# Performance work log

Measured on AMD Instinct MI355X. Metric: run time of the kernel, lower is better.

## Reference

```python
import jax, jax.numpy as jnp
import numpy as np

IMG, P, INC = 384, 2, 3
C = 2 * IMG            # embed_dim = 768
NP_ = IMG // P         # 192 patches
N = NP_ + 1            # 193 tokens with cls
L, H, E, K, B = 6, 12, 8, 2, 32
HD = C // H
EPS = 1e-5


def layer_norm(x, w, b):
    m = jnp.mean(x, -1, keepdims=True)
    v = jnp.mean((x - m) ** 2, -1, keepdims=True)
    return (x - m) * jax.lax.rsqrt(v + EPS) * w + b


def setup_inputs() -> dict:
    key = jax.random.key(0)
    ks = iter(jax.random.split(key, 32))
    nrm = lambda sh, s=0.02: jax.random.normal(next(ks), sh, jnp.float32) * s
    inp = {
        'x1': nrm((B, INC, IMG, IMG), 1.0),
        'x2': nrm((B, INC, IMG, IMG), 1.0),
        'patch_w': nrm((C, INC, IMG, P)),
        'patch_b': jnp.zeros((C,)),
        'cls_token': nrm((1, 1, C), 1e-6),
        'ln1_w': jnp.ones((L, C)), 'ln1_b': jnp.zeros((L, C)),
        'qkv_w': nrm((L, 3 * C, C)), 'qkv_b': jnp.zeros((L, 3 * C)),
        'proj_w': nrm((L, C, C)), 'proj_b': jnp.zeros((L, C)),
        'ln2_w': jnp.ones((L, C)), 'ln2_b': jnp.zeros((L, C)),
        'route_w': nrm((L, E, C)), 'route_b': jnp.zeros((L, E)),
        'rln_w': jnp.ones((L, E)), 'rln_b': jnp.zeros((L, E)),
        'expert_w': nrm((L, E, C, C)), 'expert_b': jnp.zeros((L, E, C)),
        'norm_w': jnp.ones((C,)), 'norm_b': jnp.zeros((C,)),
    }
    # fixed 1D sin-cos positional embedding (build_sincos_encoding)
    pd = C // 2
    omega = jnp.exp(jnp.arange(pd, dtype=jnp.float32) * (-np.log(10000.0) / pd))
    ow = jnp.arange(NP_, dtype=jnp.float32)[:, None] * omega
    pe = jnp.concatenate([jnp.sin(ow), jnp.cos(ow)], axis=1)          # [192, C]
    inp['pos_emb'] = jnp.concatenate([jnp.zeros((1, C)), pe], axis=0)[None]  # [1, N, C]
    return inp


def _patch_embed(x, patch_w, patch_b, cls_token, pos_emb):
    b = x.shape[0]
    # non-overlapping (IMG, P) conv == matmul on patches, flattened in (c, kh, kw) order
    xp = x.reshape(b, INC, IMG, NP_, P).transpose(0, 3, 1, 2, 4).reshape(b, NP_, INC * IMG * P)
    tok = xp @ patch_w.reshape(C, -1).T + patch_b                     # [B, 192, C]
    tok = jnp.concatenate([jnp.broadcast_to(cls_token, (b, 1, C)), tok], axis=1)
    return tok + pos_emb


def _encoder(x, view_id, ln1_w, ln1_b, qkv_w, qkv_b, proj_w, proj_b,
             ln2_w, ln2_b, route_w, route_b, rln_w, rln_b, expert_w, expert_b):
    scale = HD ** -0.5
    base = jax.random.fold_in(jax.random.key(1234), view_id)
    b = x.shape[0]

    def step(h, p):
        idx, l1w, l1b, qw, qb, pw, pb, l2w, l2b, rw, rb, rlw, rlb, ew, eb = p
        # --- attention ---
        y = layer_norm(h, l1w, l1b)
        qkv = (y @ qw.T + qb).reshape(b, N, 3, H, HD).transpose(2, 0, 3, 1, 4)
        q, k, v = qkv[0], qkv[1], qkv[2]
        a = jax.nn.softmax(jnp.einsum('bhqd,bhkd->bhqk', q, k) * scale, axis=-1)
        o = jnp.einsum('bhqk,bhkd->bhqd', a, v).transpose(0, 2, 1, 3).reshape(b, N, C)
        h = h + o @ pw.T + pb
        # --- MoE ---
        y = layer_norm(h, l2w, l2b)
        logits = layer_norm(y @ rw.T + rb, rlw, rlb)                  # [B, N, E]
        noise = jax.random.normal(jax.random.fold_in(base, idx), logits.shape) / E
        rwts = jax.nn.softmax(logits, axis=-1) + noise
        topw, topi = jax.lax.top_k(rwts, K)
        topw = jax.nn.softmax(topw, axis=-1)
        # dense all-expert compute, as in the source module
        eo = jnp.einsum('bni,eoi->bneo', y, ew) + eb                  # [B, N, E, C]
        sel = jnp.take_along_axis(eo, topi[..., None], axis=2)        # [B, N, K, C]
        h = h + (sel * topw[..., None]).sum(axis=2)
        return h, None

    xs = (jnp.arange(L), ln1_w, ln1_b, qkv_w, qkv_b, proj_w, proj_b,
          ln2_w, ln2_b, route_w, route_b, rln_w, rln_b, expert_w, expert_b)
    x, _ = jax.lax.scan(step, x, xs)
    return x


def reference(x1, x2, patch_w, patch_b, cls_token, ln1_w, ln1_b, qkv_w, qkv_b,
              proj_w, proj_b, ln2_w, ln2_b, route_w, route_b, rln_w, rln_b,
              expert_w, expert_b, norm_w, norm_b, pos_emb):
    def tower(x, vid):
        h = _patch_embed(x, patch_w, patch_b, cls_token, pos_emb)
        h = _encoder(h, vid, ln1_w, ln1_b, qkv_w, qkv_b, proj_w, proj_b,
                     ln2_w, ln2_b, route_w, route_b, rln_w, rln_b, expert_w, expert_b)
        return layer_norm(h, norm_w, norm_b)[:, 0]
    return jnp.concatenate([tower(x1, 0), tower(x2, 1)], axis=1)      # [B, 2*C]
```

## Files before the change

### kernel.cpp

```cpp
#include <hip/hip_runtime.h>
#include <stdint.h>

#define C_DIM   768
#define N_TOK   193
#define B_TOT   64
#define ROWS    (B_TOT * N_TOK)
#define QKV_DIM 2304
#define N_HEAD  12
#define N_EXP   8
#define MAXPER  ROWS
#define RTOK    64

enum { MODE_PATCH = 0, MODE_PLAIN = 1, MODE_RESID = 2, MODE_EXPERT = 3 };

typedef __attribute__((ext_vector_type(8))) short bf16x8;
typedef __attribute__((ext_vector_type(4))) float f32x4;

__device__ __forceinline__ uint32_t rotl32(uint32_t x, int n){ return (x << n) | (x >> (32 - n)); }

__device__ __forceinline__ void tf2x32(uint32_t k0, uint32_t k1, uint32_t x0, uint32_t x1,
                                       uint32_t &r0, uint32_t &r1){
  uint32_t k2 = k0 ^ k1 ^ 0x1BD11BDAu;
#define TF4(a,b,c,d) x0+=x1; x1=rotl32(x1,a); x1^=x0; x0+=x1; x1=rotl32(x1,b); x1^=x0; \
                     x0+=x1; x1=rotl32(x1,c); x1^=x0; x0+=x1; x1=rotl32(x1,d); x1^=x0;
  x0 += k0; x1 += k1;
  TF4(13,15,26, 6)  x0 += k1; x1 += k2 + 1u;
  TF4(17,29,16,24)  x0 += k2; x1 += k0 + 2u;
  TF4(13,15,26, 6)  x0 += k0; x1 += k1 + 3u;
  TF4(17,29,16,24)  x0 += k1; x1 += k2 + 4u;
  TF4(13,15,26, 6)  x0 += k2; x1 += k0 + 5u;
#undef TF4
  r0 = x0; r1 = x1;
}

__device__ __forceinline__ float jax_erfinv(float x){
  float w = -log1pf(-x * x);
  float p;
  if (w < 5.0f){
    w -= 2.5f;
    p =              2.81022636e-08f;
    p = fmaf(p, w,   3.43273939e-07f);
    p = fmaf(p, w,  -3.5233877e-06f);
    p = fmaf(p, w,  -4.39150654e-06f);
    p = fmaf(p, w,   0.00021858087f);
    p = fmaf(p, w,  -0.00125372503f);
    p = fmaf(p, w,  -0.00417768164f);
    p = fmaf(p, w,   0.246640727f);
    p = fmaf(p, w,   1.50140941f);
  } else {
    w = sqrtf(w) - 3.0f;
    p =             -0.000200214257f;
    p = fmaf(p, w,   0.000100950558f);
    p = fmaf(p, w,   0.00134934322f);
    p = fmaf(p, w,  -0.00367342844f);
    p = fmaf(p, w,   0.00573950773f);
    p = fmaf(p, w,  -0.0076224613f);
    p = fmaf(p, w,   0.00943887047f);
    p = fmaf(p, w,   1.00167406f);
    p = fmaf(p, w,   2.83297682f);
  }
  return p * x;
}

__device__ __forceinline__ float jax_noise(uint32_t c0, uint32_t c1, uint32_t j){
  uint32_t o0, o1;
  tf2x32(c0, c1, 0u, j, o0, o1);
  uint32_t bits = o0 ^ o1;
  float f = __uint_as_float(0x3f800000u | (bits >> 9)) - 1.0f;
  const float lo = -0.99999994f;
  float u = fmaxf(lo, f * 2.0f + lo);
  return 1.41421356237f * jax_erfinv(u) * 0.125f;
}

__device__ __forceinline__ unsigned short f2bf(float x){
  union { float f; uint32_t u; } v; v.f = x;
  uint32_t u = v.u;
  uint32_t r = (u + 0x7FFFu + ((u >> 16) & 1u)) >> 16;
  return (unsigned short)r;
}
__device__ __forceinline__ float bf2f(unsigned short h){
  union { uint32_t u; float f; } v; v.u = ((uint32_t)h) << 16;
  return v.f;
}

__global__ __launch_bounds__(64) void k_zero8(int* __restrict__ p){
  if ((int)threadIdx.x < N_EXP) p[threadIdx.x] = 0;
}

__global__ __launch_bounds__(64) void k_sentinel(float* __restrict__ out, float v){
  if (threadIdx.x == 0) out[0] = v;
}

__global__ __launch_bounds__(256) void k_cls(float* __restrict__ h, const float* __restrict__ cls,
                                             const float* __restrict__ pos){
  const int bt = blockIdx.x;
  #pragma unroll
  for (int u = 0; u < 3; ++u){
    int c = threadIdx.x + u * 256;
    h[(size_t)bt * N_TOK * C_DIM + c] = cls[c] + pos[c];
  }
}

__device__ __forceinline__ float blk_sum(float v, float* sb){
  #pragma unroll
  for (int off = 32; off > 0; off >>= 1) v += __shfl_down(v, off, 64);
  const int lane = threadIdx.x & 63, w = threadIdx.x >> 6;
  if (lane == 0) sb[w] = v;
  __syncthreads();
  if (threadIdx.x == 0) sb[4] = sb[0] + sb[1] + sb[2] + sb[3];
  __syncthreads();
  float r = sb[4];
  __syncthreads();
  return r;
}

__global__ __launch_bounds__(256) void k_layernorm(const float* __restrict__ x, float* __restrict__ y,
                                                   const float* __restrict__ w, const float* __restrict__ b){
  __shared__ float sb[8];
  const float* xr = x + (size_t)blockIdx.x * C_DIM;
  float v0 = xr[threadIdx.x], v1 = xr[threadIdx.x + 256], v2 = xr[threadIdx.x + 512];
  float mean = blk_sum(v0 + v1 + v2, sb) * (1.0f / 768.0f);
  float d0 = v0 - mean, d1 = v1 - mean, d2 = v2 - mean;
  float var = blk_sum(d0 * d0 + d1 * d1 + d2 * d2, sb) * (1.0f / 768.0f);
  float inv = 1.0f / sqrtf(var + 1e-5f);
  float* yr = y + (size_t)blockIdx.x * C_DIM;
  yr[threadIdx.x]       = d0 * inv * w[threadIdx.x]       + b[threadIdx.x];
  yr[threadIdx.x + 256] = d1 * inv * w[threadIdx.x + 256] + b[threadIdx.x + 256];
  yr[threadIdx.x + 512] = d2 * inv * w[threadIdx.x + 512] + b[threadIdx.x + 512];
}

__global__ __launch_bounds__(256) void k_combine_ln(
    float* __restrict__ h, const float* __restrict__ eout, const float* __restrict__ topw,
    float* __restrict__ y, const float* __restrict__ w, const float* __restrict__ b)
{
  __shared__ float sb[8];
  const int tok = blockIdx.x;
  const float w0 = topw[tok * 2], w1 = topw[tok * 2 + 1];
  const size_t hb = (size_t)tok * C_DIM;
  const size_t e0 = (size_t)(tok * 2) * C_DIM, e1 = e0 + C_DIM;
  const int t = threadIdx.x;
  float v0 = h[hb + t]       + (w0 * eout[e0 + t]       + w1 * eout[e1 + t]);
  float v1 = h[hb + t + 256] + (w0 * eout[e0 + t + 256] + w1 * eout[e1 + t + 256]);
  float v2 = h[hb + t + 512] + (w0 * eout[e0 + t + 512] + w1 * eout[e1 + t + 512]);
  h[hb + t]       = v0;
  h[hb + t + 256] = v1;
  h[hb + t + 512] = v2;
  float mean = blk_sum(v0 + v1 + v2, sb) * (1.0f / 768.0f);
  float d0 = v0 - mean, d1 = v1 - mean, d2 = v2 - mean;
  float var = blk_sum(d0 * d0 + d1 * d1 + d2 * d2, sb) * (1.0f / 768.0f);
  float inv = 1.0f / sqrtf(var + 1e-5f);
  y[hb + t]       = d0 * inv * w[t]       + b[t];
  y[hb + t + 256] = d1 * inv * w[t + 256] + b[t + 256];
  y[hb + t + 512] = d2 * inv * w[t + 512] + b[t + 512];
}

__global__ __launch_bounds__(256) void k_final(const float* __restrict__ h, float* __restrict__ out,
                                               const float* __restrict__ w, const float* __restrict__ b){
  __shared__ float sb[8];
  const int bt = blockIdx.x;
  const float* xr = h + (size_t)bt * N_TOK * C_DIM;
  float v0 = xr[threadIdx.x], v1 = xr[threadIdx.x + 256], v2 = xr[threadIdx.x + 512];
  float mean = blk_sum(v0 + v1 + v2, sb) * (1.0f / 768.0f);
  float d0 = v0 - mean, d1 = v1 - mean, d2 = v2 - mean;
  float var = blk_sum(d0 * d0 + d1 * d1 + d2 * d2, sb) * (1.0f / 768.0f);
  float inv = 1.0f / sqrtf(var + 1e-5f);
  float* orow = out + (size_t)(bt & 31) * 1536 + (size_t)(bt >> 5) * C_DIM;
  orow[threadIdx.x]       = d0 * inv * w[threadIdx.x]       + b[threadIdx.x];
  orow[threadIdx.x + 256] = d1 * inv * w[threadIdx.x + 256] + b[threadIdx.x + 256];
  orow[threadIdx.x + 512] = d2 * inv * w[threadIdx.x + 512] + b[threadIdx.x + 512];
}

template<int MODE>
__global__ __launch_bounds__(256) void k_mgemm(
    const float* __restrict__ A, const float* __restrict__ W,
    const float* __restrict__ bias, float* __restrict__ C,
    int M, int Nc, int Kc,
    const float* __restrict__ xa, const float* __restrict__ xb,
    const float* __restrict__ pos,
    const int* __restrict__ elist, const int* __restrict__ ecnt)
{
  __shared__ short sAhi[128][40];
  __shared__ short sAlo[128][40];
  __shared__ short sBhi[128][40];
  __shared__ short sBlo[128][40];

  const int tid = threadIdx.x;

  int e = 0;
  int Mloc = M;
  const float* Wp = W;
  const float* bp = bias;
  if constexpr (MODE == MODE_EXPERT){
    e = blockIdx.z;
    Mloc = ecnt[e];
    Wp = W + (size_t)e * C_DIM * C_DIM;
    bp = bias + e * C_DIM;
  }
  const int row0 = blockIdx.x * 128;
  const int col0 = blockIdx.y * 128;
  if (row0 >= Mloc) return;

  const int srow = tid >> 1;
  const int skh  = (tid & 1) * 16;

  const float* arow = A;
  bool avalid = false;
  const float* psrc = nullptr;
  if constexpr (MODE == MODE_PLAIN || MODE == MODE_RESID){
    int r = row0 + srow;
    avalid = r < Mloc;
    arow = A + (size_t)(avalid ? r : 0) * Kc;
  } else if constexpr (MODE == MODE_EXPERT){
    int r = row0 + srow;
    avalid = r < Mloc;
    if (avalid) arow = A + (size_t)(elist[e * MAXPER + r] >> 1) * C_DIM;
  } else {
    int r = row0 + srow;
    int bt = r / 192;
    int n  = r - bt * 192;
    const float* xp = (bt < 32) ? xa : xb;
    psrc = xp + (size_t)(bt & 31) * 3 * 384 * 384 + n * 2;
    avalid = true;
  }
  const float* brow = Wp + (size_t)(col0 + srow) * Kc;

  const int wv = tid >> 6;
  const int wr = (wv >> 1) * 64;
  const int wc = (wv & 1) * 64;
  const int lane = tid & 63;
  const int lrow = lane & 15;
  const int lkh  = (lane >> 4) * 8;

  f32x4 acc[4][4] = {};

  float va[16], vb[16];
  auto loadA = [&](int k0){
    if constexpr (MODE == MODE_PATCH){
      int c   = k0 / 768;
      int rem = k0 - c * 768;
      const float* pc = psrc + ((size_t)c * 384 + (rem >> 1)) * 384;
      #pragma unroll
      for (int m = 0; m < 8; ++m){
        va[m * 2 + 0] = pc[(size_t)m * 384 + 0];
        va[m * 2 + 1] = pc[(size_t)m * 384 + 1];
      }
    } else {
      if (avalid){
        *(float4*)&va[0]  = *(const float4*)(arow + k0);
        *(float4*)&va[4]  = *(const float4*)(arow + k0 + 4);
        *(float4*)&va[8]  = *(const float4*)(arow + k0 + 8);
        *(float4*)&va[12] = *(const float4*)(arow + k0 + 12);
      } else {
        #pragma unroll
        for (int j = 0; j < 16; ++j) va[j] = 0.f;
      }
    }
  };
  auto loadB = [&](int k0){
    *(float4*)&vb[0]  = *(const float4*)(brow + k0);
    *(float4*)&vb[4]  = *(const float4*)(brow + k0 + 4);
    *(float4*)&vb[8]  = *(const float4*)(brow + k0 + 8);
    *(float4*)&vb[12] = *(const float4*)(brow + k0 + 12);
  };

  loadA(skh);
  loadB(skh);

  const int nkt = Kc / 32;
  for (int kt = 0; kt < nkt; ++kt){
    {
      short hi[16], lo[16];
      #pragma unroll
      for (int j = 0; j < 16; ++j){
        unsigned short hb = f2bf(va[j]);
        hi[j] = (short)hb;
        lo[j] = (short)f2bf(va[j] - bf2f(hb));
      }
      *(bf16x8*)&sAhi[srow][skh]     = *(bf16x8*)&hi[0];
      *(bf16x8*)&sAhi[srow][skh + 8] = *(bf16x8*)&hi[8];
      *(bf16x8*)&sAlo[srow][skh]     = *(bf16x8*)&lo[0];
      *(bf16x8*)&sAlo[srow][skh + 8] = *(bf16x8*)&lo[8];
      #pragma unroll
      for (int j = 0; j < 16; ++j){
        unsigned short hb = f2bf(vb[j]);
        hi[j] = (short)hb;
        lo[j] = (short)f2bf(vb[j] - bf2f(hb));
      }
      *(bf16x8*)&sBhi[srow][skh]     = *(bf16x8*)&hi[0];
      *(bf16x8*)&sBhi[srow][skh + 8] = *(bf16x8*)&hi[8];
      *(bf16x8*)&sBlo[srow][skh]     = *(bf16x8*)&lo[0];
      *(bf16x8*)&sBlo[srow][skh + 8] = *(bf16x8*)&lo[8];
    }
    __syncthreads();
    if (kt + 1 < nkt){
      loadA((kt + 1) * 32 + skh);
      loadB((kt + 1) * 32 + skh);
    }
    bf16x8 ahi[4], alo[4], bhi[4], blo[4];
    #pragma unroll
    for (int i = 0; i < 4; ++i){
      ahi[i] = *(const bf16x8*)&sAhi[wr + i * 16 + lrow][lkh];
      alo[i] = *(const bf16x8*)&sAlo[wr + i * 16 + lrow][lkh];
    }
    #pragma unroll
    for (int j = 0; j < 4; ++j){
      bhi[j] = *(const bf16x8*)&sBhi[wc + j * 16 + lrow][lkh];
      blo[j] = *(const bf16x8*)&sBlo[wc + j * 16 + lrow][lkh];
    }
    #pragma unroll
    for (int i = 0; i < 4; ++i)
      #pragma unroll
      for (int j = 0; j < 4; ++j){
        acc[i][j] = __builtin_amdgcn_mfma_f32_16x16x32_bf16(ahi[i], bhi[j], acc[i][j], 0, 0, 0);
        acc[i][j] = __builtin_amdgcn_mfma_f32_16x16x32_bf16(ahi[i], blo[j], acc[i][j], 0, 0, 0);
        acc[i][j] = __builtin_amdgcn_mfma_f32_16x16x32_bf16(alo[i], bhi[j], acc[i][j], 0, 0, 0);
      }
    __syncthreads();
  }

  #pragma unroll
  for (int i = 0; i < 4; ++i){
    const int rbase = row0 + wr + i * 16 + (lane >> 4) * 4;
    #pragma unroll
    for (int r = 0; r < 4; ++r){
      const int rg = rbase + r;
      if (rg >= Mloc) continue;
      if constexpr (MODE == MODE_PATCH){
        int bt = rg / 192, n = rg - (rg / 192) * 192;
        size_t orow = ((size_t)bt * N_TOK + n + 1) * C_DIM;
        size_t prow = (size_t)(n + 1) * C_DIM;
        #pragma unroll
        for (int j = 0; j < 4; ++j){
          int cg = col0 + wc + j * 16 + (lane & 15);
          C[orow + cg] = acc[i][j][r] + bp[cg] + pos[prow + cg];
        }
      } else if constexpr (MODE == MODE_PLAIN){
        size_t orow = (size_t)rg * Nc;
        #pragma unroll
        for (int j = 0; j < 4; ++j){
          int cg = col0 + wc + j * 16 + (lane & 15);
          C[orow + cg] = acc[i][j][r] + bp[cg];
        }
      } else if constexpr (MODE == MODE_RESID){
        size_t orow = (size_t)rg * Nc;
        #pragma unroll
        for (int j = 0; j < 4; ++j){
          int cg = col0 + wc + j * 16 + (lane & 15);
          C[orow + cg] += acc[i][j][r] + bp[cg];
        }
      } else {
        int ts = elist[e * MAXPER + rg];
        size_t orow = (size_t)ts * C_DIM;
        #pragma unroll
        for (int j = 0; j < 4; ++j){
          int cg = col0 + wc + j * 16 + (lane & 15);
          C[orow + cg] = acc[i][j][r] + bp[cg];
        }
      }
    }
  }
}

__global__ __launch_bounds__(256) void k_attn(const float* __restrict__ qkv, float* __restrict__ o_out){
  __shared__ short sQhi[64][72],  sQlo[64][72];
  __shared__ short sKPhi[64][72], sKPlo[64][72];
  __shared__ short sVThi[64][72], sVTlo[64][72];

  const int q0 = blockIdx.x * 64;
  const int bh = blockIdx.y;
  const int bt = bh / N_HEAD, hh = bh - bt * N_HEAD;
  const int tid = threadIdx.x;
  const size_t base = (size_t)bt * N_TOK * QKV_DIM + (size_t)hh * 64;

  const int srow = tid >> 2;
  const int sk   = (tid & 3) * 16;

  {
    float v[16] = {};
    int q = q0 + srow;
    if (q < N_TOK){
      const float* src = qkv + base + (size_t)q * QKV_DIM + sk;
      *(float4*)&v[0]  = *(const float4*)(src);
      *(float4*)&v[4]  = *(const float4*)(src + 4);
      *(float4*)&v[8]  = *(const float4*)(src + 8);
      *(float4*)&v[12] = *(const float4*)(src + 12);
    }
    short hi[16], lo[16];
    #pragma unroll
    for (int j = 0; j < 16; ++j){
      unsigned short hb = f2bf(v[j]);
      hi[j] = (short)hb;
      lo[j] = (short)f2bf(v[j] - bf2f(hb));
    }
    *(bf16x8*)&sQhi[srow][sk]     = *(bf16x8*)&hi[0];
    *(bf16x8*)&sQhi[srow][sk + 8] = *(bf16x8*)&hi[8];
    *(bf16x8*)&sQlo[srow][sk]     = *(bf16x8*)&lo[0];
    *(bf16x8*)&sQlo[srow][sk + 8] = *(bf16x8*)&lo[8];
  }

  const int wv   = tid >> 6;
  const int lane = tid & 63;
  const int lrow = lane & 15;
  const int lkh  = (lane >> 4) * 8;

  f32x4 Oacc[4] = {};
  float mrun[4] = {-1e30f, -1e30f, -1e30f, -1e30f};
  float lrun[4] = {};

  for (int kt = 0; kt < 4; ++kt){
    const int n0 = kt * 64;
    __syncthreads();
    {
      float v[16] = {};
      int kk = n0 + srow;
      bool valid = kk < N_TOK;
      if (valid){
        const float* src = qkv + base + 768 + (size_t)kk * QKV_DIM + sk;
        *(float4*)&v[0]  = *(const float4*)(src);
        *(float4*)&v[4]  = *(const float4*)(src + 4);
        *(float4*)&v[8]  = *(const float4*)(src + 8);
        *(float4*)&v[12] = *(const float4*)(src + 12);
      }
      short hi[16], lo[16];
      #pragma unroll
      for (int j = 0; j < 16; ++j){
        unsigned short hb = f2bf(v[j]);
        hi[j] = (short)hb;
        lo[j] = (short)f2bf(v[j] - bf2f(hb));
      }
      *(bf16x8*)&sKPhi[srow][sk]     = *(bf16x8*)&hi[0];
      *(bf16x8*)&sKPhi[srow][sk + 8] = *(bf16x8*)&hi[8];
      *(bf16x8*)&sKPlo[srow][sk]     = *(bf16x8*)&lo[0];
      *(bf16x8*)&sKPlo[srow][sk + 8] = *(bf16x8*)&lo[8];
      float vv[16] = {};
      if (valid){
        const float* src = qkv + base + 1536 + (size_t)kk * QKV_DIM + sk;
        *(float4*)&vv[0]  = *(const float4*)(src);
        *(float4*)&vv[4]  = *(const float4*)(src + 4);
        *(float4*)&vv[8]  = *(const float4*)(src + 8);
        *(float4*)&vv[12] = *(const float4*)(src + 12);
      }
      #pragma unroll
      for (int j = 0; j < 16; ++j){
        unsigned short hb = f2bf(vv[j]);
        sVThi[sk + j][srow] = (short)hb;
        sVTlo[sk + j][srow] = (short)f2bf(vv[j] - bf2f(hb));
      }
    }
    __syncthreads();

    f32x4 s[4] = {};
    {
      bf16x8 ahi0 = *(const bf16x8*)&sQhi[wv * 16 + lrow][lkh];
      bf16x8 alo0 = *(const bf16x8*)&sQlo[wv * 16 + lrow][lkh];
      bf16x8 ahi1 = *(const bf16x8*)&sQhi[wv * 16 + lrow][32 + lkh];
      bf16x8 alo1 = *(const bf16x8*)&sQlo[wv * 16 + lrow][32 + lkh];
      #pragma unroll
      for (int j = 0; j < 4; ++j){
        bf16x8 bhi0 = *(const bf16x8*)&sKPhi[j * 16 + lrow][lkh];
        bf16x8 blo0 = *(const bf16x8*)&sKPlo[j * 16 + lrow][lkh];
        bf16x8 bhi1 = *(const bf16x8*)&sKPhi[j * 16 + lrow][32 + lkh];
        bf16x8 blo1 = *(const bf16x8*)&sKPlo[j * 16 + lrow][32 + lkh];
        s[j] = __builtin_amdgcn_mfma_f32_16x16x32_bf16(ahi0, bhi0, s[j], 0, 0, 0);
        s[j] = __builtin_amdgcn_mfma_f32_16x16x32_bf16(ahi0, blo0, s[j], 0, 0, 0);
        s[j] = __builtin_amdgcn_mfma_f32_16x16x32_bf16(alo0, bhi0, s[j], 0, 0, 0);
        s[j] = __builtin_amdgcn_mfma_f32_16x16x32_bf16(ahi1, bhi1, s[j], 0, 0, 0);
        s[j] = __builtin_amdgcn_mfma_f32_16x16x32_bf16(ahi1, blo1, s[j], 0, 0, 0);
        s[j] = __builtin_amdgcn_mfma_f32_16x16x32_bf16(alo1, bhi1, s[j], 0, 0, 0);
      }
    }
    #pragma unroll
    for (int j = 0; j < 4; ++j){
      bool masked = (n0 + j * 16 + lrow) >= N_TOK;
      #pragma unroll
      for (int r = 0; r < 4; ++r){
        s[j][r] *= 0.125f;
        if (masked) s[j][r] = -1e30f;
      }
    }

    float p[4][4], fac[4];
    #pragma unroll
    for (int r = 0; r < 4; ++r){
      float rm = fmaxf(fmaxf(s[0][r], s[1][r]), fmaxf(s[2][r], s[3][r]));
      rm = fmaxf(rm, __shfl_xor(rm, 1, 64));
      rm = fmaxf(rm, __shfl_xor(rm, 2, 64));
      rm = fmaxf(rm, __shfl_xor(rm, 4, 64));
      rm = fmaxf(rm, __shfl_xor(rm, 8, 64));
      float mn = fmaxf(mrun[r], rm);
      fac[r] = expf(mrun[r] - mn);
      mrun[r] = mn;
      lrun[r] *= fac[r];
      float rs = 0.f;
      #pragma unroll
      for (int j = 0; j < 4; ++j){ p[j][r] = expf(s[j][r] - mn); rs += p[j][r]; }
      rs += __shfl_xor(rs, 1, 64);
      rs += __shfl_xor(rs, 2, 64);
      rs += __shfl_xor(rs, 4, 64);
      rs += __shfl_xor(rs, 8, 64);
      lrun[r] += rs;
      #pragma unroll
      for (int j = 0; j < 4; ++j) Oacc[j][r] *= fac[r];
    }

    __syncthreads();
    #pragma unroll
    for (int r = 0; r < 4; ++r){
      const int prow = wv * 16 + (lane >> 4) * 4 + r;
      #pragma unroll
      for (int j = 0; j < 4; ++j){
        unsigned short hb = f2bf(p[j][r]);
        sKPhi[prow][j * 16 + lrow] = (short)hb;
        sKPlo[prow][j * 16 + lrow] = (short)f2bf(p[j][r] - bf2f(hb));
      }
    }

    {
      bf16x8 phi0 = *(const bf16x8*)&sKPhi[wv * 16 + lrow][lkh];
      bf16x8 plo0 = *(const bf16x8*)&sKPlo[wv * 16 + lrow][lkh];
      bf16x8 phi1 = *(const bf16x8*)&sKPhi[wv * 16 + lrow][32 + lkh];
      bf16x8 plo1 = *(const bf16x8*)&sKPlo[wv * 16 + lrow][32 + lkh];
      #pragma unroll
      for (int j = 0; j < 4; ++j){
        bf16x8 vhi0 = *(const bf16x8*)&sVThi[j * 16 + lrow][lkh];
        bf16x8 vlo0 = *(const bf16x8*)&sVTlo[j * 16 + lrow][lkh];
        bf16x8 vhi1 = *(const bf16x8*)&sVThi[j * 16 + lrow][32 + lkh];
        bf16x8 vlo1 = *(const bf16x8*)&sVTlo[j * 16 + lrow][32 + lkh];
        Oacc[j] = __builtin_amdgcn_mfma_f32_16x16x32_bf16(phi0, vhi0, Oacc[j], 0, 0, 0);
        Oacc[j] = __builtin_amdgcn_mfma_f32_16x16x32_bf16(phi0, vlo0, Oacc[j], 0, 0, 0);
        Oacc[j] = __builtin_amdgcn_mfma_f32_16x16x32_bf16(plo0, vhi0, Oacc[j], 0, 0, 0);
        Oacc[j] = __builtin_amdgcn_mfma_f32_16x16x32_bf16(phi1, vhi1, Oacc[j], 0, 0, 0);
        Oacc[j] = __builtin_amdgcn_mfma_f32_16x16x32_bf16(phi1, vlo1, Oacc[j], 0, 0, 0);
        Oacc[j] = __builtin_amdgcn_mfma_f32_16x16x32_bf16(plo1, vhi1, Oacc[j], 0, 0, 0);
      }
    }
  }

  #pragma unroll
  for (int r = 0; r < 4; ++r){
    int q = q0 + wv * 16 + (lane >> 4) * 4 + r;
    if (q < N_TOK){
      float inv = 1.0f / lrun[r];
      #pragma unroll
      for (int j = 0; j < 4; ++j)
        o_out[((size_t)bt * N_TOK + q) * C_DIM + hh * 64 + j * 16 + lrow] = Oacc[j][r] * inv;
    }
  }
}

__global__ __launch_bounds__(256) void k_router(
    const float* __restrict__ y, const float* __restrict__ rw, const float* __restrict__ rb,
    const float* __restrict__ rlw, const float* __restrict__ rlb,
    float* __restrict__ topw, int* __restrict__ elist, int* __restrict__ ecnt, int l)
{
  __shared__ float4 sw4[1536];
  __shared__ int lcnt[8];
  __shared__ int lbase[8];
  __shared__ int llist[8][RTOK];
  const int tid = threadIdx.x;
  const float4* rw4 = (const float4*)rw;
  #pragma unroll
  for (int u = 0; u < 6; ++u)
    sw4[tid + u * 256] = rw4[tid + u * 256];
  if (tid < 8) lcnt[tid] = 0;
  __syncthreads();

  const int wid = tid >> 6, lane = tid & 63;
  const int e = lane & 7;

  for (int t16 = 0; t16 < RTOK / 4; ++t16){
    const int tok = blockIdx.x * RTOK + wid * (RTOK / 4) + t16;
    const float4* y4 = (const float4*)(y + (size_t)tok * C_DIM);
    const float4 a0 = y4[lane], a1 = y4[64 + lane], a2 = y4[128 + lane];

    float part[8];
    #pragma unroll
    for (int ee = 0; ee < 8; ++ee){
      const float4 w0 = sw4[ee * 192 + lane];
      const float4 w1 = sw4[ee * 192 + 64 + lane];
      const float4 w2 = sw4[ee * 192 + 128 + lane];
      float s = a0.x * w0.x;
      s = fmaf(a0.y, w0.y, s); s = fmaf(a0.z, w0.z, s); s = fmaf(a0.w, w0.w, s);
      s = fmaf(a1.x, w1.x, s); s = fmaf(a1.y, w1.y, s); s = fmaf(a1.z, w1.z, s); s = fmaf(a1.w, w1.w, s);
      s = fmaf(a2.x, w2.x, s); s = fmaf(a2.y, w2.y, s); s = fmaf(a2.z, w2.z, s); s = fmaf(a2.w, w2.w, s);
      part[ee] = s;
    }
    #pragma unroll
    for (int ee = 0; ee < 8; ++ee)
      #pragma unroll
      for (int off = 32; off; off >>= 1) part[ee] += __shfl_xor(part[ee], off, 64);

    float logit = part[e] + rb[e];
    float ssum = logit;
    ssum += __shfl_xor(ssum, 1, 64); ssum += __shfl_xor(ssum, 2, 64); ssum += __shfl_xor(ssum, 4, 64);
    float mean = ssum * 0.125f;
    float d = logit - mean;
    float vs = d * d;
    vs += __shfl_xor(vs, 1, 64); vs += __shfl_xor(vs, 2, 64); vs += __shfl_xor(vs, 4, 64);
    float ln = d * (1.0f / sqrtf(vs * 0.125f + 1e-5f)) * rlw[e] + rlb[e];
    float mx = ln;
    mx = fmaxf(mx, __shfl_xor(mx, 1, 64)); mx = fmaxf(mx, __shfl_xor(mx, 2, 64)); mx = fmaxf(mx, __shfl_xor(mx, 4, 64));
    float ex = expf(ln - mx);
    float es = ex;
    es += __shfl_xor(es, 1, 64); es += __shfl_xor(es, 2, 64); es += __shfl_xor(es, 4, 64);
    float prob = ex / es;
    int t = tok / 6176;
    int rem = tok - t * 6176;
    int b = rem / N_TOK, n = rem - (rem / N_TOK) * N_TOK;
    uint32_t b0, b1, c0, c1;
    tf2x32(0u, 1234u, 0u, (uint32_t)t, b0, b1);
    tf2x32(b0, b1, 0u, (uint32_t)l, c0, c1);
    uint32_t j = (uint32_t)(b * N_TOK + n) * 8u + (uint32_t)e;
    float r = prob + jax_noise(c0, c1, j);
    float v1 = r; int i1 = e;
    #pragma unroll
    for (int off = 1; off <= 4; off <<= 1){
      float ov = __shfl_xor(v1, off, 64); int oi = __shfl_xor(i1, off, 64);
      if (ov > v1 || (ov == v1 && oi < i1)){ v1 = ov; i1 = oi; }
    }
    float rm2 = (e == i1) ? -3.0e38f : r;
    float v2 = rm2; int i2 = e;
    #pragma unroll
    for (int off = 1; off <= 4; off <<= 1){
      float ov = __shfl_xor(v2, off, 64); int oi = __shfl_xor(i2, off, 64);
      if (ov > v2 || (ov == v2 && oi < i2)){ v2 = ov; i2 = oi; }
    }
    float e2 = expf(v2 - v1);
    float sum = 1.0f + e2;
    if (lane == 0){
      topw[tok * 2 + 0] = 1.0f / sum;
      topw[tok * 2 + 1] = e2 / sum;
      int p = atomicAdd(&lcnt[i1], 1);
      llist[i1][p] = tok * 2;
      int p2 = atomicAdd(&lcnt[i2], 1);
      llist[i2][p2] = tok * 2 + 1;
    }
  }
  __syncthreads();
  if (tid < 8) lbase[tid] = atomicAdd(&ecnt[tid], lcnt[tid]);
  __syncthreads();
  #pragma unroll
  for (int ee = 0; ee < 8; ++ee){
    const int cnt = lcnt[ee];
    const int bse = lbase[ee];
    for (int i = tid; i < cnt; i += 256)
      elist[ee * MAXPER + bse + i] = llist[ee][i];
  }
}

__global__ __launch_bounds__(256) void k_combine(float* __restrict__ h, const float* __restrict__ eout,
                                                 const float* __restrict__ topw){
  const int tok = blockIdx.x;
  const float w0 = topw[tok * 2], w1 = topw[tok * 2 + 1];
  const size_t hb = (size_t)tok * C_DIM;
  const size_t e0 = (size_t)(tok * 2) * C_DIM, e1 = e0 + C_DIM;
  #pragma unroll
  for (int u = 0; u < 3; ++u){
    int c = threadIdx.x + u * 256;
    h[hb + c] += w0 * eout[e0 + c] + w1 * eout[e1 + c];
  }
}

extern "C" void kernel_launch(void* const* d_in, const int* in_sizes, int n_in,
                              void* d_out, int out_size, void* d_ws, size_t ws_size,
                              hipStream_t stream){
  float* out = (float*)d_out;

  static const int kExp[22] = {
    14155776, 14155776, 1769472, 768, 768,
    4608, 4608, 10616832, 13824, 3538944, 4608,
    4608, 4608, 36864, 48, 48, 48,
    28311552, 36864, 768, 768, 148224};
  const size_t need_f = (size_t)ROWS * C_DIM * 2 + (size_t)ROWS * QKV_DIM
                      + (size_t)ROWS * 2 + (size_t)N_EXP * MAXPER + 8;
  float bad = 0.f;
  if (n_in != 22) bad = 2.0e6f;
  else {
    for (int i = 0; i < 22; ++i)
      if (in_sizes[i] != kExp[i]){ bad = 4.0e6f + i * 1.0e4f; break; }
  }
  if (bad == 0.f && out_size != 49152) bad = 3.0e6f;
  if (bad == 0.f && ws_size < need_f * 4) bad = 1.0e6f;
  if (bad != 0.f){
    k_sentinel<<<dim3(1), 64, 0, stream>>>(out, bad);
    return;
  }

  const float* x1       = (const float*)d_in[0];
  const float* x2       = (const float*)d_in[1];
  const float* patch_w  = (const float*)d_in[2];
  const float* patch_b  = (const float*)d_in[3];
  const float* cls_tok  = (const float*)d_in[4];
  const float* ln1_w    = (const float*)d_in[5];
  const float* ln1_b    = (const float*)d_in[6];
  const float* qkv_w    = (const float*)d_in[7];
  const float* qkv_b    = (const float*)d_in[8];
  const float* proj_w   = (const float*)d_in[9];
  const float* proj_b   = (const float*)d_in[10];
  const float* ln2_w    = (const float*)d_in[11];
  const float* ln2_b    = (const float*)d_in[12];
  const float* route_w  = (const float*)d_in[13];
  const float* route_b  = (const float*)d_in[14];
  const float* rln_w    = (const float*)d_in[15];
  const float* rln_b    = (const float*)d_in[16];
  const float* expert_w = (const float*)d_in[17];
  const float* expert_b = (const float*)d_in[18];
  const float* norm_w   = (const float*)d_in[19];
  const float* norm_b   = (const float*)d_in[20];
  const float* pos_emb  = (const float*)d_in[21];

  float* ws = (float*)d_ws;
  size_t off = 0;
  float* h    = ws + off; off += (size_t)ROWS * C_DIM;
  float* y    = ws + off; off += (size_t)ROWS * C_DIM;
  float* qkv  = ws + off; off += (size_t)ROWS * QKV_DIM;
  float* eout = qkv;
  float* topw = ws + off; off += (size_t)ROWS * 2;
  int*   elist = (int*)(ws + off); off += (size_t)N_EXP * MAXPER;
  int*   ecnt  = (int*)(ws + off); off += 8;

  k_cls<<<dim3(B_TOT), 256, 0, stream>>>(h, cls_tok, pos_emb);
  k_mgemm<MODE_PATCH><<<dim3(96, 6), 256, 0, stream>>>(
      nullptr, patch_w, patch_b, h, 12288, C_DIM, 2304, x1, x2, pos_emb, nullptr, nullptr);

  k_layernorm<<<dim3(ROWS), 256, 0, stream>>>(h, y, ln1_w, ln1_b);
  for (int l = 0; l < 6; ++l){
    k_mgemm<MODE_PLAIN><<<dim3(97, 18), 256, 0, stream>>>(
        y, qkv_w + (size_t)l * QKV_DIM * C_DIM, qkv_b + l * QKV_DIM, qkv,
        ROWS, QKV_DIM, C_DIM, nullptr, nullptr, nullptr, nullptr, nullptr);
    k_attn<<<dim3(4, B_TOT * N_HEAD), 256, 0, stream>>>(qkv, y);
    k_mgemm<MODE_RESID><<<dim3(97, 6), 256, 0, stream>>>(
        y, proj_w + (size_t)l * C_DIM * C_DIM, proj_b + l * C_DIM, h,
        ROWS, C_DIM, C_DIM, nullptr, nullptr, nullptr, nullptr, nullptr);
    k_layernorm<<<dim3(ROWS), 256, 0, stream>>>(h, y, ln2_w + l * C_DIM, ln2_b + l * C_DIM);
    k_zero8<<<dim3(1), 64, 0, stream>>>(ecnt);
    k_router<<<dim3(ROWS / RTOK), 256, 0, stream>>>(
        y, route_w + (size_t)l * N_EXP * C_DIM, route_b + l * N_EXP,
        rln_w + l * N_EXP, rln_b + l * N_EXP, topw, elist, ecnt, l);
    k_mgemm<MODE_EXPERT><<<dim3(97, 6, N_EXP), 256, 0, stream>>>(
        y, expert_w + (size_t)l * N_EXP * C_DIM * C_DIM, expert_b + (size_t)l * N_EXP * C_DIM, eout,
        ROWS, C_DIM, C_DIM, nullptr, nullptr, nullptr, elist, ecnt);
    if (l < 5){
      k_combine_ln<<<dim3(ROWS), 256, 0, stream>>>(
          h, eout, topw, y, ln1_w + (l + 1) * C_DIM, ln1_b + (l + 1) * C_DIM);
    } else {
      k_combine<<<dim3(ROWS), 256, 0, stream>>>(h, eout, topw);
    }
  }
  k_final<<<dim3(B_TOT), 256, 0, stream>>>(h, out, norm_w, norm_b);
}
```

Before: 3.822 ms.

## Double-buffer split-bf16 GEMM shared tiles and use truncation for high part

Shared-memory tiles in the split-bf16 MFMA GEMM become double-buffered. The next tile is converted and stored into the alternate buffer while the current one is consumed, and global loads are prefetched two tiles ahead, which removes one barrier per K step. The hi/lo split now takes the high part by truncation instead of round-to-nearest, so the conversion is cheaper. The lo residual still captures the remainder. This doubles LDS use, which may lower occupancy, and changes the rounding split slightly.

```diff
diff --git a/kernel.cpp b/kernel.cpp
--- a/kernel.cpp
+++ b/kernel.cpp
@@ -82,6 +82,13 @@
   union { uint32_t u; float f; } v; v.u = ((uint32_t)h) << 16;
   return v.f;
 }
+__device__ __forceinline__ void fsplit_t(float x, short &hi, short &lo){
+  union { float f; uint32_t u; } v; v.f = x;
+  uint32_t hb = v.u & 0xFFFF0000u;
+  hi = (short)(hb >> 16);
+  union { uint32_t u; float f; } hv; hv.u = hb;
+  lo = (short)f2bf(x - hv.f);
+}
 
 __global__ __launch_bounds__(64) void k_zero8(int* __restrict__ p){
   if ((int)threadIdx.x < N_EXP) p[threadIdx.x] = 0;
@@ -179,10 +186,10 @@
     const float* __restrict__ pos,
     const int* __restrict__ elist, const int* __restrict__ ecnt)
 {
-  __shared__ short sAhi[128][40];
-  __shared__ short sAlo[128][40];
-  __shared__ short sBhi[128][40];
-  __shared__ short sBlo[128][40];
+  __shared__ short sAhi[2][128][40];
+  __shared__ short sAlo[2][128][40];
+  __shared__ short sBhi[2][128][40];
+  __shared__ short sBlo[2][128][40];
 
   const int tid = threadIdx.x;
 
@@ -262,50 +269,47 @@
     *(float4*)&vb[8]  = *(const float4*)(brow + k0 + 8);
     *(float4*)&vb[12] = *(const float4*)(brow + k0 + 12);
   };
-
-  loadA(skh);
-  loadB(skh);
+  auto cvstore = [&](int buf){
+    short hi[16], lo[16];
+    #pragma unroll
+    for (int j = 0; j < 16; ++j) fsplit_t(va[j], hi[j], lo[j]);
+    *(bf16x8*)&sAhi[buf][srow][skh]     = *(bf16x8*)&hi[0];
+    *(bf16x8*)&sAhi[buf][srow][skh + 8] = *(bf16x8*)&hi[8];
+    *(bf16x8*)&sAlo[buf][srow][skh]     = *(bf16x8*)&lo[0];
+    *(bf16x8*)&sAlo[buf][srow][skh + 8] = *(bf16x8*)&lo[8];
+    #pragma unroll
+    for (int j = 0; j < 16; ++j) fsplit_t(vb[j], hi[j], lo[j]);
+    *(bf16x8*)&sBhi[buf][srow][skh]     = *(bf16x8*)&hi[0];
+    *(bf16x8*)&sBhi[buf][srow][skh + 8] = *(bf16x8*)&hi[8];
+    *(bf16x8*)&sBlo[buf][srow][skh]     = *(bf16x8*)&lo[0];
+    *(bf16x8*)&sBlo[buf][srow][skh + 8] = *(bf16x8*)&lo[8];
+  };
 
   const int nkt = Kc / 32;
+  loadA(skh); loadB(skh);
+  cvstore(0);
+  loadA(32 + skh); loadB(32 + skh);
+  __syncthreads();
+
   for (int kt = 0; kt < nkt; ++kt){
-    {
-      short hi[16], lo[16];
-      #pragma unroll
-      for (int j = 0; j < 16; ++j){
-        unsigned short hb = f2bf(va[j]);
-        hi[j] = (short)hb;
-        lo[j] = (short)f2bf(va[j] - bf2f(hb));
-      }
-      *(bf16x8*)&sAhi[srow][skh]     = *(bf16x8*)&hi[0];
-      *(bf16x8*)&sAhi[srow][skh + 8] = *(bf16x8*)&hi[8];
-      *(bf16x8*)&sAlo[srow][skh]     = *(bf16x8*)&lo[0];
-      *(bf16x8*)&sAlo[srow][skh + 8] = *(bf16x8*)&lo[8];
-      #pragma unroll
-      for (int j = 0; j < 16; ++j){
-        unsigned short hb = f2bf(vb[j]);
-        hi[j] = (short)hb;
-        lo[j] = (short)f2bf(vb[j] - bf2f(hb));
-      }
-      *(bf16x8*)&sBhi[srow][skh]     = *(bf16x8*)&hi[0];
-      *(bf16x8*)&sBhi[srow][skh + 8] = *(bf16x8*)&hi[8];
-      *(bf16x8*)&sBlo[srow][skh]     = *(bf16x8*)&lo[0];
-      *(bf16x8*)&sBlo[srow][skh + 8] = *(bf16x8*)&lo[8];
-    }
-    __syncthreads();
+    const int cur = kt & 1;
+    bf16x8 ahi[4], alo[4], bhi[4], blo[4];
+    #pragma unroll
+    for (int i = 0; i < 4; ++i){
+      ahi[i] = *(const bf16x8*)&sAhi[cur][wr + i * 16 + lrow][lkh];
+      alo[i] = *(const bf16x8*)&sAlo[cur][wr + i * 16 + lrow][lkh];
+    }
+    #pragma unroll
+    for (int j = 0; j < 4; ++j){
+      bhi[j] = *(const bf16x8*)&sBhi[cur][wc + j * 16 + lrow][lkh];
+      blo[j] = *(const bf16x8*)&sBlo[cur][wc + j * 16 + lrow][lkh];
+    }
     if (kt + 1 < nkt){
-      loadA((kt + 1) * 32 + skh);
-      loadB((kt + 1) * 32 + skh);
-    }
-    bf16x8 ahi[4], alo[4], bhi[4], blo[4];
-    #pragma unroll
-    for (int i = 0; i < 4; ++i){
-      ahi[i] = *(const bf16x8*)&sAhi[wr + i * 16 + lrow][lkh];
-      alo[i] = *(const bf16x8*)&sAlo[wr + i * 16 + lrow][lkh];
-    }
-    #pragma unroll
-    for (int j = 0; j < 4; ++j){
-      bhi[j] = *(const bf16x8*)&sBhi[wc + j * 16 + lrow][lkh];
-      blo[j] = *(const bf16x8*)&sBlo[wc + j * 16 + lrow][lkh];
+      cvstore(cur ^ 1);
+      if (kt + 2 < nkt){
+        loadA((kt + 2) * 32 + skh);
+        loadB((kt + 2) * 32 + skh);
+      }
     }
     #pragma unroll
     for (int i = 0; i < 4; ++i)
```

New measurement: 4.501 ms. +17.8%, slower.
